# Kernel optimization log

Hardware: AMD Instinct MI355X
Metric: run time of the kernel (lower is better)

Reference implementation:

```python
import jax, jax.numpy as jnp
import numpy as np

N_HEAD = 16
N_KV_HEAD = 8
HEAD_DIM = 128
BLOCK_SIZE = 2048


def _rope_cache(T, hd):
    # faithful to torch: freqs repeat_interleave(2) along last dim
    inv_freq = 1.0 / (10000.0 ** (jnp.arange(0, hd, 2, dtype=jnp.float32) / hd))
    t = jnp.arange(T, dtype=jnp.float32)
    freqs = jnp.outer(t, inv_freq)            # [T, hd/2]
    freqs = jnp.repeat(freqs, 2, axis=-1)     # [T, hd]
    return jnp.cos(freqs), jnp.sin(freqs)


def _apply_rope(x, cos, sin):
    # x: [B, H, T, hd]; rotate-half convention from the torch code
    hd = x.shape[-1]
    x1, x2 = x[..., : hd // 2], x[..., hd // 2 :]
    x_rot = jnp.concatenate([-x2, x1], axis=-1)
    return x * cos + x_rot * sin


def setup_inputs() -> dict:
    key = jax.random.key(0)
    ks = jax.random.split(key, 5)
    B, T, C = 4, 2048, 2048
    kv_dim = N_KV_HEAD * HEAD_DIM
    s = 0.02
    return {
        "x": jax.random.normal(ks[0], (B, T, C), dtype=jnp.float32),
        "Wq": jax.random.normal(ks[1], (C, C), dtype=jnp.float32) * s,
        "Wk": jax.random.normal(ks[2], (kv_dim, C), dtype=jnp.float32) * s,
        "Wv": jax.random.normal(ks[3], (kv_dim, C), dtype=jnp.float32) * s,
        "Wo": jax.random.normal(ks[4], (C, C), dtype=jnp.float32) * s,
    }


def reference(x, Wq, Wk, Wv, Wo):
    B, T, C = x.shape
    hd = HEAD_DIM
    # projections (torch Linear: x @ W.T)
    q = (x @ Wq.T).reshape(B, T, N_HEAD, hd).transpose(0, 2, 1, 3)      # [B,H,T,hd]
    k = (x @ Wk.T).reshape(B, T, N_KV_HEAD, hd).transpose(0, 2, 1, 3)   # [B,Hkv,T,hd]
    v = (x @ Wv.T).reshape(B, T, N_KV_HEAD, hd).transpose(0, 2, 1, 3)

    cos, sin = _rope_cache(T, hd)  # start_pos = 0
    q = _apply_rope(q, cos, sin)
    k = _apply_rope(k, cos, sin)

    # GQA: repeat kv heads
    rep = N_HEAD // N_KV_HEAD
    k = jnp.repeat(k, rep, axis=1)  # [B,H,T,hd]
    v = jnp.repeat(v, rep, axis=1)

    scale = 1.0 / jnp.sqrt(jnp.float32(hd))
    scores = jnp.einsum("bhqd,bhkd->bhqk", q, k) * scale
    causal = jnp.tril(jnp.ones((T, T), dtype=bool))
    scores = jnp.where(causal, scores, jnp.finfo(scores.dtype).min)
    attn = jax.nn.softmax(scores, axis=-1)
    out = jnp.einsum("bhqk,bhkd->bhqd", attn, v)  # [B,H,T,hd]

    y = out.transpose(0, 2, 1, 3).reshape(B, T, C)
    return y @ Wo.T
```

## Files before the change

kernel.cpp:

```cpp
#include <hip/hip_runtime.h>

#define SCALE 0.08838834764831845f

typedef unsigned short bfu;
typedef __attribute__((ext_vector_type(8))) short bf16x8;
typedef __attribute__((ext_vector_type(4))) float f32x4;
typedef __attribute__((ext_vector_type(16))) float f32x16;

__device__ __forceinline__ unsigned short f2bf(float f) {
  unsigned int u = __float_as_uint(f);
  u += 0x7FFFu + ((u >> 16) & 1u);
  return (unsigned short)(u >> 16);
}
__device__ __forceinline__ float bf2f(unsigned short h) {
  return __uint_as_float(((unsigned int)h) << 16);
}
__device__ __forceinline__ unsigned int cvtpk(float a, float b) {
  unsigned int r;
  asm("v_cvt_pk_bf16_f32 %0, %1, %2" : "=v"(r) : "v"(a), "v"(b));
  return r;
}
__device__ __forceinline__ void pl32swap(unsigned int& a, unsigned int& b) {
  asm volatile("v_permlane32_swap_b32 %0, %1" : "+v"(a), "+v"(b));
}
__device__ __forceinline__ void async16(const void* g, void* l) {
  __builtin_amdgcn_global_load_lds(
      (const __attribute__((address_space(1))) unsigned int*)g,
      (__attribute__((address_space(3))) unsigned int*)l, 16, 0, 0);
}
__device__ __forceinline__ void barrier_sb() {
  __builtin_amdgcn_sched_barrier(0);
  __builtin_amdgcn_s_barrier();
  __builtin_amdgcn_sched_barrier(0);
}
__device__ __forceinline__ void wait0_bar() {
  __builtin_amdgcn_sched_barrier(0);
  asm volatile("s_waitcnt vmcnt(0)" ::: "memory");
  __builtin_amdgcn_s_barrier();
  __builtin_amdgcn_sched_barrier(0);
}

__global__ __launch_bounds__(256) void cvt_bf16(const float* __restrict__ src,
                                                bfu* __restrict__ dst, int n4) {
  int i = blockIdx.x * 256 + threadIdx.x;
  if (i >= n4) return;
  float4 v = ((const float4*)src)[i];
  ushort4 o;
  o.x = f2bf(v.x); o.y = f2bf(v.y); o.z = f2bf(v.z); o.w = f2bf(v.w);
  ((ushort4*)dst)[i] = o;
}

__global__ __launch_bounds__(256) void rope_table(float2* __restrict__ tab) {
  int idx = blockIdx.x * 256 + threadIdx.x;
  int t = idx >> 6, f = idx & 63;
  const float nl = -0.14391156463f;
  float th = (float)t * expf((float)f * nl);
  tab[idx] = make_float2(cosf(th), sinf(th));
}

__device__ __forceinline__ void storeC(float* p, float v) { *p = v; }
__device__ __forceinline__ void storeC(bfu* p, float v) { *p = f2bf(v); }

template <typename OutT, bool FUSE>
__global__ __launch_bounds__(512, 2) void gemm256(
    const bfu* __restrict__ A, const bfu* __restrict__ B,
    OutT* __restrict__ C, const float2* __restrict__ ropeTab,
    bfu* __restrict__ qTo, bfu* __restrict__ kTo, bfu* __restrict__ vTo,
    int M, int N, int K) {
  __shared__ __align__(16) char smem[131072];
  const int tid = threadIdx.x;
  const int w = tid >> 6, l = tid & 63;
  const int lr = l & 15, lg = l >> 4;
  const int wr = w >> 2, wc = w & 3;

  const int nwg = gridDim.x * gridDim.y;
  const int flat = blockIdx.y * gridDim.x + blockIdx.x;
  const int swz = (flat & 7) * (nwg >> 3) + (flat >> 3);
  const int m0 = (swz % gridDim.x) * 256;
  const int n0 = (swz / gridDim.x) * 256;

  const int sr = l >> 3;
  const int sc = (l & 7) ^ sr;
  auto stageHalf = [&](const bfu* G, int grow0, int kcol, char* lds) {
#pragma unroll
    for (int j = 0; j < 2; j++) {
      int row = (j * 8 + w) * 8 + sr;
      async16(G + (size_t)(grow0 + row) * K + kcol + sc * 8,
              lds + (j * 8 + w) * 1024 + l * 16);
    }
  };

  f32x4 acc[8][4];
#pragma unroll
  for (int i = 0; i < 8; i++)
#pragma unroll
    for (int j = 0; j < 4; j++) acc[i][j] = (f32x4){0.f, 0.f, 0.f, 0.f};

  stageHalf(A, m0, 0, smem);
  stageHalf(A, m0 + 128, 0, smem + 16384);
  stageHalf(B, n0, 0, smem + 65536);
  stageHalf(B, n0 + 128, 0, smem + 65536 + 16384);

  const int KT = K >> 6;
  const int swiz = (lr & 7) << 4;
  const int cbase = (wc >> 1) * 128 + (wc & 1) * 32;
#pragma unroll 1
  for (int t = 0; t < KT; t++) {
    const int bt = t & 1;
    const char* Ah = smem + bt * 32768 + wr * 16384;
    const char* Bt = smem + 65536 + bt * 32768;
    char* An = smem + (bt ^ 1) * 32768;
    char* Bn = smem + 65536 + (bt ^ 1) * 32768;
    const bool pfch = (t + 1 < KT);
    const int kn = (t + 1) << 6;

    if (pfch) {
      stageHalf(A, m0, kn, An);
      asm volatile("s_waitcnt vmcnt(2)" ::: "memory");
    } else {
      asm volatile("s_waitcnt vmcnt(0)" ::: "memory");
    }
    barrier_sb();

    bf16x8 bfr[4][2];
#pragma unroll
    for (int n = 0; n < 4; n++) {
      const char* rowp =
          Bt + (cbase + (n & 1) * 16 + (n >> 1) * 64 + lr) * 128;
#pragma unroll
      for (int s = 0; s < 2; s++)
        bfr[n][s] = *(const bf16x8*)(rowp + ((((s << 2) + lg) << 4) ^ swiz));
    }

#pragma unroll
    for (int p = 0; p < 4; p++) {
      bf16x8 af[2][2];
#pragma unroll
      for (int m2 = 0; m2 < 2; m2++) {
        const char* rowp = Ah + ((p * 2 + m2) * 16 + lr) * 128;
#pragma unroll
        for (int s = 0; s < 2; s++)
          af[m2][s] = *(const bf16x8*)(rowp + ((((s << 2) + lg) << 4) ^ swiz));
      }
      if (pfch) {
        if (p == 1) stageHalf(A, m0 + 128, kn, An + 16384);
        if (p == 2) stageHalf(B, n0, kn, Bn);
        if (p == 3) stageHalf(B, n0 + 128, kn, Bn + 16384);
      }
      __builtin_amdgcn_s_setprio(1);
#pragma unroll
      for (int m2 = 0; m2 < 2; m2++)
#pragma unroll
        for (int n = 0; n < 4; n++)
#pragma unroll
          for (int s = 0; s < 2; s++)
            acc[p * 2 + m2][n] = __builtin_amdgcn_mfma_f32_16x16x32_bf16(
                af[m2][s], bfr[n][s], acc[p * 2 + m2][n], 0, 0, 0);
      __builtin_amdgcn_s_setprio(0);
    }
    barrier_sb();
  }

  if constexpr (!FUSE) {
#pragma unroll
    for (int i = 0; i < 8; i++)
#pragma unroll
      for (int j = 0; j < 4; j++)
#pragma unroll
        for (int r = 0; r < 4; r++) {
          int gm = m0 + wr * 128 + i * 16 + lg * 4 + r;
          int gn = n0 + cbase + (j & 1) * 16 + (j >> 1) * 64 + lr;
          storeC(&C[(size_t)gm * N + gn], acc[i][j][r]);
        }
  } else {
    const int head = (n0 >> 7) + (wc >> 1);
    if (head < 24) {
#pragma unroll
      for (int i = 0; i < 8; i++)
#pragma unroll
        for (int r = 0; r < 4; r++) {
          int gm = m0 + wr * 128 + i * 16 + lg * 4 + r;
          int tt = gm & 2047, bb = gm >> 11;
          bfu* rowp = (head < 16)
                          ? qTo + (((size_t)((bb * 16 + head) * 2048 + tt)) << 7)
                          : kTo + (((size_t)((bb * 8 + head - 16) * 2048 + tt)) << 7);
          const float2* trow = ropeTab + tt * 64;
#pragma unroll
          for (int n = 0; n < 2; n++) {
            int d = (wc & 1) * 32 + n * 16 + lr;
            int i1 = d >> 1;
            float2 cs1 = trow[i1];
            float2 cs2 = trow[i1 + 32];
            float x1 = acc[i][n][r], x2 = acc[i][n + 2][r];
            rowp[d] = f2bf(x1 * cs1.x - x2 * cs1.y);
            rowp[d + 64] = f2bf(x2 * cs2.x + x1 * cs2.y);
          }
        }
    } else {
      const int kh = head - 24;
#pragma unroll
      for (int i = 0; i < 8; i++) {
        int gm0 = m0 + wr * 128 + i * 16 + lg * 4;
        int t0 = gm0 & 2047, bb = gm0 >> 11;
#pragma unroll
        for (int n = 0; n < 4; n++) {
          int d = (wc & 1) * 32 + (n & 1) * 16 + (n >> 1) * 64 + lr;
          bfu* p = vTo + (((size_t)((bb * 8 + kh) * 128 + d)) << 11) + t0;
          ushort4 o;
          o.x = f2bf(acc[i][n][0]);
          o.y = f2bf(acc[i][n][1]);
          o.z = f2bf(acc[i][n][2]);
          o.w = f2bf(acc[i][n][3]);
          *(ushort4*)p = o;
        }
      }
    }
  }
}

__global__ __launch_bounds__(512, 2) void flash_attn7(const bfu* __restrict__ qT,
                                                      const bfu* __restrict__ kT,
                                                      const bfu* __restrict__ vT,
                                                      bfu* __restrict__ attn) {
  __shared__ __align__(16) char smem[65536];
  const int tid = threadIdx.x;
  const int w = tid >> 6, l = tid & 63;
  const int ln = l & 31, h2 = l >> 5;
  const int hsw = w >> 2, w4 = w & 3;
  const int idx = blockIdx.x;
  const int khb = idx & 31;
  const int pg = idx >> 5;
  const int kh = khb & 7, b = khb >> 3;
  const int hh = kh * 2 + hsw;
  const int nkbA = 2 * pg + 2;
  const int NT = 34;

  const bfu* Qh = qT + ((size_t)(b * 16 + hh) * 2048) * 128;
  const bfu* Kb = kT + ((size_t)(b * 8 + kh) * 2048) * 128;
  const bfu* Vb = vT + ((size_t)(b * 8 + kh) * 128) * 2048;

  auto stageK = [&](int buf, int t) {
    char* Kl = smem + buf * 16384;
    const bfu* src = Kb + (size_t)t * 64 * 128;
#pragma unroll
    for (int ii = 0; ii < 2; ii++) {
      int i = w * 2 + ii;
      int row = i * 4 + (l >> 4);
      int ck = (l & 15) ^ (row & 15);
      async16(src + row * 128 + ck * 8, Kl + i * 1024 + l * 16);
    }
  };
  auto stageV = [&](int buf, int t) {
    char* Vl = smem + 32768 + buf * 16384;
    const bfu* src = Vb + t * 64;
#pragma unroll
    for (int jj = 0; jj < 2; jj++) {
      int j = w * 2 + jj;
      int row = j * 8 + (l >> 3);
      int ck = (l & 7) ^ (row & 7);
      async16(src + (size_t)row * 2048 + ck * 8, Vl + j * 1024 + l * 16);
    }
  };

  int qrow0 = pg * 128 + w4 * 32;

  bf16x8 qf[8];
#pragma unroll
  for (int dt = 0; dt < 8; dt++)
    qf[dt] = *(const bf16x8*)(Qh + (size_t)(qrow0 + ln) * 128 + dt * 16 + h2 * 8);

  f32x16 O[4];
#pragma unroll
  for (int mt = 0; mt < 4; mt++)
#pragma unroll
    for (int r = 0; r < 16; r++) O[mt][r] = 0.f;
  float li = 0.f;

  auto flush = [&]() {
    float ls = li + __shfl_xor(li, 32);
    float inv = 1.f / ls;
    bfu* orow = attn + ((size_t)(b * 2048 + qrow0 + ln)) * 2048 + hh * 128;
#pragma unroll
    for (int mt = 0; mt < 4; mt++)
#pragma unroll
      for (int g = 0; g < 4; g++) {
        unsigned int r0 = cvtpk(O[mt][g * 4 + 0] * inv, O[mt][g * 4 + 1] * inv);
        unsigned int r1 = cvtpk(O[mt][g * 4 + 2] * inv, O[mt][g * 4 + 3] * inv);
        uint2 o; o.x = r0; o.y = r1;
        *(uint2*)(orow + mt * 32 + g * 8 + h2 * 4) = o;
      }
  };

  stageK(0, 0);
  stageV(0, 0);

#pragma unroll 1
  for (int t = 0; t < NT; t++) {
    wait0_bar();
    if (t + 1 < NT) {
      const int kn = (t + 1 >= nkbA) ? (t + 1 - nkbA) : (t + 1);
      stageK((t + 1) & 1, kn);
      stageV((t + 1) & 1, kn);
    }

    if (t == nkbA) {
      flush();
      qrow0 = (15 - pg) * 128 + w4 * 32;
#pragma unroll
      for (int dt = 0; dt < 8; dt++)
        qf[dt] =
            *(const bf16x8*)(Qh + (size_t)(qrow0 + ln) * 128 + dt * 16 + h2 * 8);
#pragma unroll
      for (int mt = 0; mt < 4; mt++)
#pragma unroll
        for (int r = 0; r < 16; r++) O[mt][r] = 0.f;
      li = 0.f;
    }

    const int k0 = ((t >= nkbA) ? (t - nkbA) : t) * 64;
    const int myrow = qrow0 + ln;
    if (k0 <= qrow0 + 31) {
      const char* Kl = smem + (t & 1) * 16384;
      const char* Vl = smem + 32768 + (t & 1) * 16384;

      f32x16 S0, S1;
#pragma unroll
      for (int r = 0; r < 16; r++) { S0[r] = 0.f; S1[r] = 0.f; }
      const int swk = (ln & 15) << 4;
      __builtin_amdgcn_s_setprio(1);
#pragma unroll
      for (int dt = 0; dt < 8; dt++) {
        bf16x8 kf0 =
            *(const bf16x8*)(Kl + ln * 256 + ((dt * 32 + h2 * 16) ^ swk));
        bf16x8 kf1 = *(const bf16x8*)(Kl + (32 + ln) * 256 +
                                      ((dt * 32 + h2 * 16) ^ swk));
        S0 = __builtin_amdgcn_mfma_f32_32x32x16_bf16(kf0, qf[dt], S0, 0, 0, 0);
        S1 = __builtin_amdgcn_mfma_f32_32x32x16_bf16(kf1, qf[dt], S1, 0, 0, 0);
      }
      __builtin_amdgcn_s_setprio(0);

      const bool need_mask = (k0 + 63) > qrow0;
      bf16x8 pfr[4];
#pragma unroll
      for (int half = 0; half < 2; half++) {
        float p[16];
#pragma unroll
        for (int r = 0; r < 16; r++) {
          float s = half ? S1[r] : S0[r];
          float pv = __builtin_exp2f(fmaf(s, 0.12751743f, -17.312340f));
          if (need_mask) {
            int key = k0 + half * 32 + (r & 3) + 8 * (r >> 2) + 4 * h2;
            if (key > myrow) pv = 0.f;
          }
          p[r] = pv;
          li += pv;
        }
#pragma unroll
        for (int kt = 0; kt < 2; kt++) {
          const float* q = p + kt * 8;
          unsigned int a0 = cvtpk(q[0], q[1]);
          unsigned int a1 = cvtpk(q[2], q[3]);
          unsigned int b0 = cvtpk(q[4], q[5]);
          unsigned int b1 = cvtpk(q[6], q[7]);
          pl32swap(a0, b0);
          pl32swap(a1, b1);
          union { unsigned int u[4]; bf16x8 v; } c;
          c.u[0] = a0; c.u[1] = a1; c.u[2] = b0; c.u[3] = b1;
          pfr[half * 2 + kt] = c.v;
        }
      }

      const int swv = (ln & 7) << 4;
      __builtin_amdgcn_s_setprio(1);
#pragma unroll
      for (int mt = 0; mt < 4; mt++) {
        const char* vb = Vl + (mt * 32 + ln) * 128;
#pragma unroll
        for (int kt = 0; kt < 4; kt++) {
          bf16x8 vf = *(const bf16x8*)(vb + ((kt * 32 + h2 * 16) ^ swv));
          O[mt] = __builtin_amdgcn_mfma_f32_32x32x16_bf16(vf, pfr[kt], O[mt], 0, 0, 0);
        }
      }
      __builtin_amdgcn_s_setprio(0);
    }
  }

  flush();
}

extern "C" void kernel_launch(void* const* d_in, const int* in_sizes, int n_in,
                              void* d_out, int out_size, void* d_ws, size_t ws_size,
                              hipStream_t stream) {
  const float* x = (const float*)d_in[0];
  const float* Wq = (const float*)d_in[1];
  const float* Wk = (const float*)d_in[2];
  const float* Wv = (const float*)d_in[3];
  const float* Wo = (const float*)d_in[4];
  float* out = (float*)d_out;
  char* ws = (char*)d_ws;

  bfu* xb     = (bfu*)(ws);
  bfu* Wqkv   = (bfu*)(ws + 33554432);
  bfu* Wob    = (bfu*)(ws + 50331648);
  float2* tab = (float2*)(ws + 58720256);
  bfu* qT     = (bfu*)(ws + 125829120);
  bfu* kT     = (bfu*)(ws + 159383552);
  bfu* vT     = (bfu*)(ws + 176160768);
  bfu* attn = xb;

  cvt_bf16<<<16384, 256, 0, stream>>>(x, xb, 4194304);
  cvt_bf16<<<4096, 256, 0, stream>>>(Wq, Wqkv, 1048576);
  cvt_bf16<<<2048, 256, 0, stream>>>(Wk, Wqkv + (size_t)2048 * 2048, 524288);
  cvt_bf16<<<2048, 256, 0, stream>>>(Wv, Wqkv + (size_t)3072 * 2048, 524288);
  cvt_bf16<<<4096, 256, 0, stream>>>(Wo, Wob, 1048576);
  rope_table<<<512, 256, 0, stream>>>(tab);

  gemm256<bfu, true><<<dim3(32, 16), 512, 0, stream>>>(
      xb, Wqkv, (bfu*)nullptr, tab, qT, kT, vT, 8192, 4096, 2048);
  flash_attn7<<<256, 512, 0, stream>>>(qT, kT, vT, attn);
  gemm256<float, false><<<dim3(32, 8), 512, 0, stream>>>(
      attn, Wob, out, nullptr, nullptr, nullptr, nullptr, 8192, 2048, 2048);
}
```

Baseline: 453.5 us.

## Remap GEMM tiles into per-XCD regions and restructure K-loop prefetch with more barriers

Replaces the simple XCD-round-robin swizzle with a mapping that gives each XCD a contiguous region of tiles (RM rows by 4 columns), aiming for better L2 reuse of A and B panels within an XCD. The K-loop is also reorganised: both A halves are prefetched up front, both B halves are issued after the first compute phase, and barriers are added between compute phases to keep waves in lockstep. The extra barriers add synchronisation cost, and the region mapping assumes the grid dimensions divide evenly.

```diff
diff --git a/kernel.cpp b/kernel.cpp
--- a/kernel.cpp
+++ b/kernel.cpp
@@ -73,20 +73,22 @@
   const int lr = l & 15, lg = l >> 4;
   const int wr = w >> 2, wc = w & 3;
 
-  const int nwg = gridDim.x * gridDim.y;
-  const int flat = blockIdx.y * gridDim.x + blockIdx.x;
-  const int swz = (flat & 7) * (nwg >> 3) + (flat >> 3);
-  const int m0 = (swz % gridDim.x) * 256;
-  const int n0 = (swz / gridDim.x) * 256;
+  const int nm = gridDim.x, nn = gridDim.y;
+  const int flat = blockIdx.y * nm + blockIdx.x;
+  const int xcd = flat & 7, j = flat >> 3;
+  const int RM = (nm * nn) >> 5;
+  const int nregm = nm / RM;
+  const int m0 = ((xcd % nregm) * RM + (j >> 2)) * 256;
+  const int n0 = ((xcd / nregm) * 4 + (j & 3)) * 256;
 
   const int sr = l >> 3;
   const int sc = (l & 7) ^ sr;
   auto stageHalf = [&](const bfu* G, int grow0, int kcol, char* lds) {
 #pragma unroll
-    for (int j = 0; j < 2; j++) {
-      int row = (j * 8 + w) * 8 + sr;
+    for (int jj = 0; jj < 2; jj++) {
+      int row = (jj * 8 + w) * 8 + sr;
       async16(G + (size_t)(grow0 + row) * K + kcol + sc * 8,
-              lds + (j * 8 + w) * 1024 + l * 16);
+              lds + (jj * 8 + w) * 1024 + l * 16);
     }
   };
 
@@ -94,7 +96,7 @@
 #pragma unroll
   for (int i = 0; i < 8; i++)
 #pragma unroll
-    for (int j = 0; j < 4; j++) acc[i][j] = (f32x4){0.f, 0.f, 0.f, 0.f};
+    for (int jj = 0; jj < 4; jj++) acc[i][jj] = (f32x4){0.f, 0.f, 0.f, 0.f};
 
   stageHalf(A, m0, 0, smem);
   stageHalf(A, m0 + 128, 0, smem + 16384);
@@ -114,15 +116,17 @@
     const bool pfch = (t + 1 < KT);
     const int kn = (t + 1) << 6;
 
+    bf16x8 bfr[4][2];
+
     if (pfch) {
       stageHalf(A, m0, kn, An);
-      asm volatile("s_waitcnt vmcnt(2)" ::: "memory");
+      stageHalf(A, m0 + 128, kn, An + 16384);
+      asm volatile("s_waitcnt vmcnt(4)" ::: "memory");
     } else {
       asm volatile("s_waitcnt vmcnt(0)" ::: "memory");
     }
     barrier_sb();
 
-    bf16x8 bfr[4][2];
 #pragma unroll
     for (int n = 0; n < 4; n++) {
       const char* rowp =
@@ -131,9 +135,30 @@
       for (int s = 0; s < 2; s++)
         bfr[n][s] = *(const bf16x8*)(rowp + ((((s << 2) + lg) << 4) ^ swiz));
     }
-
-#pragma unroll
-    for (int p = 0; p < 4; p++) {
+    {
+      bf16x8 af[2][2];
+#pragma unroll
+      for (int m2 = 0; m2 < 2; m2++) {
+        const char* rowp = Ah + ((0 * 2 + m2) * 16 + lr) * 128;
+#pragma unroll
+        for (int s = 0; s < 2; s++)
+          af[m2][s] = *(const bf16x8*)(rowp + ((((s << 2) + lg) << 4) ^ swiz));
+      }
+      __builtin_amdgcn_s_setprio(1);
+#pragma unroll
+      for (int m2 = 0; m2 < 2; m2++)
+#pragma unroll
+        for (int n = 0; n < 4; n++)
+#pragma unroll
+          for (int s = 0; s < 2; s++)
+            acc[m2][n] = __builtin_amdgcn_mfma_f32_16x16x32_bf16(
+                af[m2][s], bfr[n][s], acc[m2][n], 0, 0, 0);
+      __builtin_amdgcn_s_setprio(0);
+    }
+    barrier_sb();
+
+#pragma unroll
+    for (int p = 1; p < 4; p++) {
       bf16x8 af[2][2];
 #pragma unroll
       for (int m2 = 0; m2 < 2; m2++) {
@@ -142,11 +167,11 @@
         for (int s = 0; s < 2; s++)
           af[m2][s] = *(const bf16x8*)(rowp + ((((s << 2) + lg) << 4) ^ swiz));
       }
-      if (pfch) {
-        if (p == 1) stageHalf(A, m0 + 128, kn, An + 16384);
-        if (p == 2) stageHalf(B, n0, kn, Bn);
-        if (p == 3) stageHalf(B, n0 + 128, kn, Bn + 16384);
-      }
+      if (p == 1 && pfch) {
+        stageHalf(B, n0, kn, Bn);
+        stageHalf(B, n0 + 128, kn, Bn + 16384);
+      }
+      barrier_sb();
       __builtin_amdgcn_s_setprio(1);
 #pragma unroll
       for (int m2 = 0; m2 < 2; m2++)
@@ -157,20 +182,20 @@
             acc[p * 2 + m2][n] = __builtin_amdgcn_mfma_f32_16x16x32_bf16(
                 af[m2][s], bfr[n][s], acc[p * 2 + m2][n], 0, 0, 0);
       __builtin_amdgcn_s_setprio(0);
-    }
-    barrier_sb();
+      barrier_sb();
+    }
   }
 
   if constexpr (!FUSE) {
 #pragma unroll
     for (int i = 0; i < 8; i++)
 #pragma unroll
-      for (int j = 0; j < 4; j++)
+      for (int jj = 0; jj < 4; jj++)
 #pragma unroll
         for (int r = 0; r < 4; r++) {
           int gm = m0 + wr * 128 + i * 16 + lg * 4 + r;
-          int gn = n0 + cbase + (j & 1) * 16 + (j >> 1) * 64 + lr;
-          storeC(&C[(size_t)gm * N + gn], acc[i][j][r]);
+          int gn = n0 + cbase + (jj & 1) * 16 + (jj >> 1) * 64 + lr;
+          storeC(&C[(size_t)gm * N + gn], acc[i][jj][r]);
         }
   } else {
     const int head = (n0 >> 7) + (wc >> 1);
```

Result: slower. 464.3 us (+2.4%).
